# Optimization experiments

Measured on AMD Instinct MI355X. Metric: run time of the kernel, lower is better.

The kernel has to match this reference:

```python
import jax, jax.numpy as jnp
import numpy as np


def setup_inputs() -> dict:
    key = jax.random.key(0)
    k1, k2, k3, k4 = jax.random.split(key, 4)
    B, S, K, N = 2, 1024, 4096, 4096
    x = jax.random.normal(k1, (B, S, K), dtype=jnp.float32)
    # int8 weights in [-128, 127]
    weight = jax.random.randint(k2, (N, K), -128, 128, dtype=jnp.int8)
    # per-output-channel dequant scales (small positive values)
    scales = jax.random.uniform(k3, (N,), dtype=jnp.float32, minval=0.005, maxval=0.02)
    bias = jax.random.normal(k4, (N,), dtype=jnp.float32) * 0.1
    return {"x": x, "weight": weight, "scales": scales, "bias": bias}


def reference(x, weight, scales, bias):
    # F.linear(x, weight.to(x.dtype)): [B,S,K] @ [N,K]^T -> [B,S,N]
    w = weight.astype(x.dtype)
    y = jnp.einsum('bsk,nk->bsn', x, w)
    # per-output-channel scale + bias epilogue
    return y * scales + bias
```

## Files before the change

kernel.cpp:

```cpp
#include <hip/hip_runtime.h>
#include <hip/hip_bf16.h>
#include <stdint.h>

#define M_DIM 2048
#define N_DIM 4096
#define K_DIM 4096

#define BM 128
#define BN 128
#define BK 128

#define ATILE (BM * BK)
#define BTILE (BN * BK)

typedef __attribute__((ext_vector_type(4))) int   int4v;
typedef __attribute__((ext_vector_type(4))) float f32x4;

__device__ __forceinline__ void load_lds16(const void* g, void* l) {
    __builtin_amdgcn_global_load_lds(
        (const __attribute__((address_space(1))) void*)g,
        (__attribute__((address_space(3))) void*)l,
        16, 0, 0);
}

__global__ __launch_bounds__(256) void quant_x(const float* __restrict__ x,
                                               int8_t* __restrict__ Aq,
                                               float* __restrict__ sx) {
    const int row = blockIdx.x;
    const int tid = threadIdx.x;
    const float4* xr = (const float4*)(x + (size_t)row * K_DIM);

    float4 v[4];
    float mx = 0.f;
#pragma unroll
    for (int p = 0; p < 4; p++) {
        v[p] = xr[p * 256 + tid];
        mx = fmaxf(mx, fmaxf(fmaxf(fabsf(v[p].x), fabsf(v[p].y)),
                             fmaxf(fabsf(v[p].z), fabsf(v[p].w))));
    }
#pragma unroll
    for (int off = 32; off >= 1; off >>= 1)
        mx = fmaxf(mx, __shfl_xor(mx, off, 64));

    __shared__ float wmax[4];
    __shared__ float smax;
    if ((tid & 63) == 0) wmax[tid >> 6] = mx;
    __syncthreads();
    if (tid == 0) {
        float m = fmaxf(fmaxf(wmax[0], wmax[1]), fmaxf(wmax[2], wmax[3]));
        m = fmaxf(m, 1e-20f);
        smax = m;
        sx[row] = m * (1.0f / 127.0f);
    }
    __syncthreads();
    const float inv = 127.0f / smax;

    int* out = (int*)Aq + (size_t)row * (K_DIM / 4);
#pragma unroll
    for (int p = 0; p < 4; p++) {
        int q0 = (int)__builtin_rintf(v[p].x * inv);
        int q1 = (int)__builtin_rintf(v[p].y * inv);
        int q2 = (int)__builtin_rintf(v[p].z * inv);
        int q3 = (int)__builtin_rintf(v[p].w * inv);
        q0 = max(-127, min(127, q0)); q1 = max(-127, min(127, q1));
        q2 = max(-127, min(127, q2)); q3 = max(-127, min(127, q3));
        out[p * 256 + tid] = (q0 & 255) | ((q1 & 255) << 8) |
                             ((q2 & 255) << 16) | ((q3 & 255) << 24);
    }
}

__global__ __launch_bounds__(256) void cvt_w8(const int* __restrict__ w,
                                              int8_t* __restrict__ Bq) {
    size_t i = ((size_t)blockIdx.x * 256 + threadIdx.x) * 16;
    int4 a0 = *(const int4*)(w + i);
    int4 a1 = *(const int4*)(w + i + 4);
    int4 a2 = *(const int4*)(w + i + 8);
    int4 a3 = *(const int4*)(w + i + 12);
    uint4 t;
    t.x = (a0.x & 255) | ((a0.y & 255) << 8) | ((a0.z & 255) << 16) | ((a0.w & 255) << 24);
    t.y = (a1.x & 255) | ((a1.y & 255) << 8) | ((a1.z & 255) << 16) | ((a1.w & 255) << 24);
    t.z = (a2.x & 255) | ((a2.y & 255) << 8) | ((a2.z & 255) << 16) | ((a2.w & 255) << 24);
    t.w = (a3.x & 255) | ((a3.y & 255) << 8) | ((a3.z & 255) << 16) | ((a3.w & 255) << 24);
    *(uint4*)(Bq + i) = t;
}


__global__ __launch_bounds__(256, 2) void gemm_bt_i8(
    const int8_t* __restrict__ A,
    const int8_t* __restrict__ B,
    const float*  __restrict__ sx,
    const float*  __restrict__ scales,
    const float*  __restrict__ bias,
    float* __restrict__ C)
{
    __shared__ __align__(16) int8_t As[2 * ATILE];
    __shared__ __align__(16) int8_t Bs[2 * BTILE];

    const int tid  = threadIdx.x;
    const int bm   = blockIdx.y;
    const int bn   = blockIdx.x;
    const int lane = tid & 63;
    const int wave = tid >> 6;
    const int wm   = (wave >> 1) * 64;
    const int wn   = (wave & 1) * 64;
    const int l16  = lane & 15;
    const int quad = lane >> 4;
    const int swz  = l16 & 7;

    const int srow = tid >> 3;
    const int cgp  = tid & 7;
    const int cgl  = cgp ^ (srow & 7);

    const int8_t* ga[4];
    const int8_t* gb[4];
#pragma unroll
    for (int s = 0; s < 4; s++) {
        ga[s] = A + (size_t)(bm * BM + s * 32 + srow) * K_DIM + cgl * 16;
        gb[s] = B + (size_t)(bn * BN + s * 32 + srow) * K_DIM + cgl * 16;
    }
    const int la = tid * 16;

#pragma unroll
    for (int s = 0; s < 4; s++) {
        load_lds16(ga[s], As + s * 4096 + la);
        load_lds16(gb[s], Bs + s * 4096 + la);
    }

    int4v acc[4][4] = {};

    int cur = 0;
    for (int k0 = 0; k0 < K_DIM; k0 += BK, cur ^= 1) {
        __syncthreads();

        const int kn = k0 + BK;
        if (kn < K_DIM) {
            const int nb = (cur ^ 1);
#pragma unroll
            for (int s = 0; s < 4; s++) {
                load_lds16(ga[s] + kn, As + nb * ATILE + s * 4096 + la);
                load_lds16(gb[s] + kn, Bs + nb * BTILE + s * 4096 + la);
            }
        }

        const int8_t* Ab = As + cur * ATILE;
        const int8_t* Bb = Bs + cur * BTILE;

#pragma unroll
        for (int h = 0; h < 2; h++) {
            const int cp = (h * 4 + quad) ^ swz;
            int4v af[4], bfr[4];
#pragma unroll
            for (int i = 0; i < 4; i++)
                af[i] = *(const int4v*)(Ab + (wm + i * 16 + l16) * BK + cp * 16);
#pragma unroll
            for (int j = 0; j < 4; j++)
                bfr[j] = *(const int4v*)(Bb + (wn + j * 16 + l16) * BK + cp * 16);
#pragma unroll
            for (int i = 0; i < 4; i++)
#pragma unroll
                for (int j = 0; j < 4; j++)
                    acc[i][j] = __builtin_amdgcn_mfma_i32_16x16x64_i8(
                        af[i], bfr[j], acc[i][j], 0, 0, 0);
        }
    }

    float sxr[16];
#pragma unroll
    for (int i = 0; i < 4; i++)
#pragma unroll
        for (int r = 0; r < 4; r++)
            sxr[i * 4 + r] = sx[bm * BM + wm + i * 16 + quad * 4 + r];

#pragma unroll
    for (int j = 0; j < 4; j++) {
        const int col = bn * BN + wn + j * 16 + l16;
        const float s = scales[col];
        const float b = bias[col];
#pragma unroll
        for (int i = 0; i < 4; i++) {
            const int row0 = bm * BM + wm + i * 16 + quad * 4;
#pragma unroll
            for (int r = 0; r < 4; r++) {
                C[(size_t)(row0 + r) * N_DIM + col] =
                    (float)acc[i][j][r] * (sxr[i * 4 + r] * s) + b;
            }
        }
    }
}


extern "C" void kernel_launch(void* const* d_in, const int* in_sizes, int n_in,
                              void* d_out, int out_size, void* d_ws, size_t ws_size,
                              hipStream_t stream) {
    const float* x      = (const float*)d_in[0];
    const int*   w      = (const int*)d_in[1];
    const float* scales = (const float*)d_in[2];
    const float* bias   = (const float*)d_in[3];
    float*       out    = (float*)d_out;

    int8_t* Aq = (int8_t*)d_ws;
    int8_t* Bq = (int8_t*)d_ws + (size_t)M_DIM * K_DIM;
    float*  sx = (float*)((int8_t*)d_ws + (size_t)(M_DIM + N_DIM) * K_DIM);

    quant_x<<<M_DIM, 256, 0, stream>>>(x, Aq, sx);
    cvt_w8<<<(int)((size_t)N_DIM * K_DIM / 16 / 256), 256, 0, stream>>>(w, Bq);

    dim3 grid(N_DIM / BN, M_DIM / BM);
    gemm_bt_i8<<<grid, 256, 0, stream>>>(Aq, Bq, sx, scales, bias, out);
}
```

Baseline: 168.7 us.

## Use 128x256 tiles with 3-stage LDS pipeline and XCD-aware block mapping

Enlarges the output tile to 128x256 with 8 waves per block, replaces double buffering with a three-slot async LDS pipeline gated by explicit vmcnt waits and raw barriers, and raises wave priority around MFMA bursts. Blocks are remapped so tiles sharing A/B rows land on the same XCD for better L2 reuse. The aim is to hide global load latency and cut redundant memory traffic. Larger LDS use (144KB) limits occupancy to one block per CU.

```diff
diff --git a/kernel.cpp b/kernel.cpp
--- a/kernel.cpp
+++ b/kernel.cpp
@@ -7,11 +7,14 @@
 #define K_DIM 4096
 
 #define BM 128
-#define BN 128
+#define BN 256
 #define BK 128
 
-#define ATILE (BM * BK)
-#define BTILE (BN * BK)
+#define NSLOT 3
+#define ASLOT (BM * BK)
+#define BSLOT (BN * BK)
+
+#define NT (K_DIM / BK)
 
 typedef __attribute__((ext_vector_type(4))) int   int4v;
 typedef __attribute__((ext_vector_type(4))) float f32x4;
@@ -85,7 +88,7 @@
 }
 
 
-__global__ __launch_bounds__(256, 2) void gemm_bt_i8(
+__global__ __launch_bounds__(512, 2) void gemm_bt_i8(
     const int8_t* __restrict__ A,
     const int8_t* __restrict__ B,
     const float*  __restrict__ sx,
@@ -93,16 +96,21 @@
     const float*  __restrict__ bias,
     float* __restrict__ C)
 {
-    __shared__ __align__(16) int8_t As[2 * ATILE];
-    __shared__ __align__(16) int8_t Bs[2 * BTILE];
+    __shared__ __align__(16) int8_t As[NSLOT * ASLOT];
+    __shared__ __align__(16) int8_t Bs[NSLOT * BSLOT];
 
     const int tid  = threadIdx.x;
-    const int bm   = blockIdx.y;
-    const int bn   = blockIdx.x;
+
+    const int bid   = blockIdx.x;
+    const int xcd   = bid & 7;
+    const int local = bid >> 3;
+    const int bm    = (xcd >> 2) * 8 + (local >> 2);
+    const int bn    = (xcd & 3) * 4 + (local & 3);
+
     const int lane = tid & 63;
     const int wave = tid >> 6;
-    const int wm   = (wave >> 1) * 64;
-    const int wn   = (wave & 1) * 64;
+    const int wm   = (wave >> 2) * 64;
+    const int wn   = (wave & 3) * 64;
     const int l16  = lane & 15;
     const int quad = lane >> 4;
     const int swz  = l16 & 7;
@@ -111,58 +119,69 @@
     const int cgp  = tid & 7;
     const int cgl  = cgp ^ (srow & 7);
 
-    const int8_t* ga[4];
-    const int8_t* gb[4];
-#pragma unroll
-    for (int s = 0; s < 4; s++) {
-        ga[s] = A + (size_t)(bm * BM + s * 32 + srow) * K_DIM + cgl * 16;
-        gb[s] = B + (size_t)(bn * BN + s * 32 + srow) * K_DIM + cgl * 16;
-    }
+    const int8_t* ga = A + (size_t)(bm * BM + srow) * K_DIM + cgl * 16;
+    const int8_t* gb = B + (size_t)(bn * BN + srow) * K_DIM + cgl * 16;
     const int la = tid * 16;
 
-#pragma unroll
-    for (int s = 0; s < 4; s++) {
-        load_lds16(ga[s], As + s * 4096 + la);
-        load_lds16(gb[s], Bs + s * 4096 + la);
-    }
+#define STAGE(slot, koff) do {                                               \
+        load_lds16(ga + (koff),                 As + (slot) * ASLOT + la);   \
+        load_lds16(ga + 64 * K_DIM + (koff),    As + (slot) * ASLOT + 8192 + la); \
+        load_lds16(gb + (koff),                 Bs + (slot) * BSLOT + la);   \
+        load_lds16(gb + 64 * K_DIM + (koff),    Bs + (slot) * BSLOT + 8192 + la); \
+        load_lds16(gb + 128 * K_DIM + (koff),   Bs + (slot) * BSLOT + 16384 + la); \
+        load_lds16(gb + 192 * K_DIM + (koff),   Bs + (slot) * BSLOT + 24576 + la); \
+    } while (0)
 
     int4v acc[4][4] = {};
 
-    int cur = 0;
-    for (int k0 = 0; k0 < K_DIM; k0 += BK, cur ^= 1) {
-        __syncthreads();
-
-        const int kn = k0 + BK;
-        if (kn < K_DIM) {
-            const int nb = (cur ^ 1);
-#pragma unroll
-            for (int s = 0; s < 4; s++) {
-                load_lds16(ga[s] + kn, As + nb * ATILE + s * 4096 + la);
-                load_lds16(gb[s] + kn, Bs + nb * BTILE + s * 4096 + la);
-            }
-        }
-
-        const int8_t* Ab = As + cur * ATILE;
-        const int8_t* Bb = Bs + cur * BTILE;
-
-#pragma unroll
-        for (int h = 0; h < 2; h++) {
-            const int cp = (h * 4 + quad) ^ swz;
-            int4v af[4], bfr[4];
-#pragma unroll
-            for (int i = 0; i < 4; i++)
-                af[i] = *(const int4v*)(Ab + (wm + i * 16 + l16) * BK + cp * 16);
-#pragma unroll
-            for (int j = 0; j < 4; j++)
-                bfr[j] = *(const int4v*)(Bb + (wn + j * 16 + l16) * BK + cp * 16);
-#pragma unroll
-            for (int i = 0; i < 4; i++)
-#pragma unroll
-                for (int j = 0; j < 4; j++)
-                    acc[i][j] = __builtin_amdgcn_mfma_i32_16x16x64_i8(
-                        af[i], bfr[j], acc[i][j], 0, 0, 0);
-        }
-    }
+#define COMPUTE(slot) do {                                                   \
+        const int8_t* Ab = As + (slot) * ASLOT;                              \
+        const int8_t* Bb = Bs + (slot) * BSLOT;                              \
+        _Pragma("unroll")                                                    \
+        for (int h = 0; h < 2; h++) {                                        \
+            const int cp = (h * 4 + quad) ^ swz;                             \
+            int4v af[4], bfr[4];                                             \
+            _Pragma("unroll")                                                \
+            for (int i = 0; i < 4; i++)                                      \
+                af[i] = *(const int4v*)(Ab + (wm + i * 16 + l16) * BK + cp * 16); \
+            _Pragma("unroll")                                                \
+            for (int j = 0; j < 4; j++)                                      \
+                bfr[j] = *(const int4v*)(Bb + (wn + j * 16 + l16) * BK + cp * 16); \
+            __builtin_amdgcn_s_setprio(1);                                   \
+            _Pragma("unroll")                                                \
+            for (int i = 0; i < 4; i++)                                      \
+                _Pragma("unroll")                                            \
+                for (int j = 0; j < 4; j++)                                  \
+                    acc[i][j] = __builtin_amdgcn_mfma_i32_16x16x64_i8(       \
+                        af[i], bfr[j], acc[i][j], 0, 0, 0);                  \
+            __builtin_amdgcn_s_setprio(0);                                   \
+        }                                                                    \
+    } while (0)
+
+    STAGE(0, 0);
+    STAGE(1, BK);
+
+    int s0 = 0, s1 = 1, s2 = 2;
+
+    for (int t = 0; t < NT - 2; ++t) {
+        asm volatile("s_waitcnt vmcnt(6)" ::: "memory");
+        __builtin_amdgcn_s_barrier();
+        STAGE(s2, (t + 2) * BK);
+        COMPUTE(s0);
+        const int tmp = s0; s0 = s1; s1 = s2; s2 = tmp;
+    }
+
+    asm volatile("s_waitcnt vmcnt(6)" ::: "memory");
+    __builtin_amdgcn_s_barrier();
+    COMPUTE(s0);
+    { const int tmp = s0; s0 = s1; s1 = s2; s2 = tmp; }
+
+    asm volatile("s_waitcnt vmcnt(0)" ::: "memory");
+    __builtin_amdgcn_s_barrier();
+    COMPUTE(s0);
+
+#undef STAGE
+#undef COMPUTE
 
     float sxr[16];
 #pragma unroll
@@ -205,6 +224,5 @@
     quant_x<<<M_DIM, 256, 0, stream>>>(x, Aq, sx);
     cvt_w8<<<(int)((size_t)N_DIM * K_DIM / 16 / 256), 256, 0, stream>>>(w, Bq);
 
-    dim3 grid(N_DIM / BN, M_DIM / BM);
-    gemm_bt_i8<<<grid, 256, 0, stream>>>(Aq, Bq, sx, scales, bias, out);
-}
+    gemm_bt_i8<<<256, 512, 0, stream>>>(Aq, Bq, sx, scales, bias, out);
+}
```

Measured after the change: 175.3 us. 3.9% more time.
